# Performance work log

Measured on AMD Instinct MI355X. Metric: run time of the kernel, lower is better.

## Reference

```python
import jax, jax.numpy as jnp
import numpy as np

WS, OWS, NHEAD = 4, 6, 6          # window, overlap window = 4 + int(0.5*4), heads
B, CIN, COU, H, W = 2, 192, 192, 224, 224
MID = CIN  # r = 1


def calc_rpi_oca(ws=WS, ows=OWS):
    # relative position index between ws x ws query window and ows x ows overlapping kv window
    co = np.stack(np.meshgrid(np.arange(ws), np.arange(ws), indexing='ij')).reshape(2, -1)
    ce = np.stack(np.meshgrid(np.arange(ows), np.arange(ows), indexing='ij')).reshape(2, -1)
    rel = (ce[:, None, :] - co[:, :, None]).transpose(1, 2, 0) + (ws - 1)  # [ws*ws, ows*ows, 2], >= 0
    idx = rel[..., 0] * (ws + ows - 1) + rel[..., 1]                       # in [0, (ws+ows-1)^2)
    return jnp.asarray(idx)  # [16, 36]

RPI = calc_rpi_oca()


def conv2d(x, w, b, pad):
    out = jax.lax.conv_general_dilated(x, w, (1, 1), [(pad, pad), (pad, pad)],
                                       dimension_numbers=('NCHW', 'OIHW', 'NCHW'))
    return out + b[None, :, None, None]


def group_norm(x, g, b, groups, eps=1e-5):
    n = x.shape[0]
    xg = x.reshape(n, groups, -1)
    mu = xg.mean(-1, keepdims=True)
    var = xg.var(-1, keepdims=True)
    xn = ((xg - mu) * jax.lax.rsqrt(var + eps)).reshape(x.shape)
    return xn * g[None, :, None, None] + b[None, :, None, None]


def layer_norm(x, g, b, eps=1e-5):
    mu = x.mean(-1, keepdims=True)
    var = x.var(-1, keepdims=True)
    return (x - mu) * jax.lax.rsqrt(var + eps) * g + b


def ocab(x, h, w, ln1_g, ln1_b, qkv_w, qkv_b, rpb, proj_w, proj_b,
         ln2_g, ln2_b, fc1_w, fc1_b, fc2_w, fc2_b):
    b, _, c = x.shape
    nh, nw, d = h // WS, w // WS, c // NHEAD
    shortcut = x
    xn = layer_norm(x, ln1_g, ln1_b).reshape(b, h, w, c)
    qkv = xn @ qkv_w + qkv_b                                  # [b,h,w,3c] laid out [q|k|v]
    q = qkv[..., :c]
    kv = jnp.stack([qkv[..., c:2 * c], qkv[..., 2 * c:]])     # [2,b,h,w,c]
    # non-overlapping query windows -> [b*nwin, 16, NHEAD, d]
    qw = q.reshape(b, nh, WS, nw, WS, c).transpose(0, 1, 3, 2, 4, 5).reshape(b * nh * nw, WS * WS, NHEAD, d)
    # overlapping kv windows = Unfold(kernel=OWS, stride=WS, pad=(OWS-WS)//2)
    pad = (OWS - WS) // 2
    kvp = jnp.pad(kv, ((0, 0), (0, 0), (pad, pad), (pad, pad), (0, 0)))
    rows = (jnp.arange(nh) * WS)[:, None] + jnp.arange(OWS)[None, :]   # [nh, OWS]
    cols = (jnp.arange(nw) * WS)[:, None] + jnp.arange(OWS)[None, :]   # [nw, OWS]
    patches = kvp[:, :, rows[:, None, :, None], cols[None, :, None, :], :]  # [2,b,nh,nw,OWS,OWS,c]
    kvw = patches.reshape(2, b * nh * nw, OWS * OWS, NHEAD, d)
    kw, vw = kvw[0], kvw[1]
    attn = jnp.einsum('wqhd,wkhd->whqk', qw * (d ** -0.5), kw)  # [b*nwin, NHEAD, 16, 36]
    bias = rpb[RPI.reshape(-1)].reshape(WS * WS, OWS * OWS, NHEAD).transpose(2, 0, 1)
    attn = jax.nn.softmax(attn + bias[None], axis=-1)
    out = jnp.einsum('whqk,wkhd->wqhd', attn, vw).reshape(b, nh, nw, WS, WS, c)
    out = out.transpose(0, 1, 3, 2, 4, 5).reshape(b, h * w, c)  # window_reverse
    out = out @ proj_w + proj_b + shortcut
    xm = layer_norm(out, ln2_g, ln2_b)
    mlp = jax.nn.gelu(xm @ fc1_w + fc1_b, approximate=False) @ fc2_w + fc2_b
    return out + mlp


def atoca_forward(x, conv1_w, conv1_b, gn1_g, gn1_b, conv2_w, conv2_b, gn2_g, gn2_b,
                  conv3_w, conv3_b, ln1_g, ln1_b, qkv_w, qkv_b, rpb, proj_w, proj_b,
                  ln2_g, ln2_b, fc1_w, fc1_b, fc2_w, fc2_b):
    Bx, C, Hx, Wx = x.shape
    shortcut = x
    # raw row-major reshape, exactly as the torch code (not a spatial window partition)
    out = x.reshape(Bx * (Hx // WS) * (Wx // WS), C, WS, WS)
    out = conv2d(out, conv1_w, conv1_b, 1)
    out = jax.nn.silu(group_norm(out, gn1_g, gn1_b, NHEAD))
    out = out.transpose(0, 2, 3, 1).reshape(Bx, Hx * Wx, -1)
    out = ocab(out, Hx, Wx, ln1_g, ln1_b, qkv_w, qkv_b, rpb, proj_w, proj_b,
               ln2_g, ln2_b, fc1_w, fc1_b, fc2_w, fc2_b)
    out = out.reshape(Bx * (Hx // WS) * (Wx // WS), WS, WS, -1).transpose(0, 3, 1, 2)
    out = conv2d(out, conv2_w, conv2_b, 1)
    out = group_norm(out, gn2_g, gn2_b, NHEAD)
    out = out.reshape(Bx, -1, Hx, Wx)
    out = out + conv2d(shortcut, conv3_w, conv3_b, 0)
    return jax.nn.relu(out)


def setup_inputs() -> dict:
    key = jax.random.key(0)
    ks = iter(jax.random.split(key, 32))
    rn = lambda shape, s=0.02: (s * jax.random.normal(next(ks), shape)).astype(jnp.float32)
    return {
        'x': jax.random.normal(next(ks), (B, CIN, H, W), dtype=jnp.float32),
        'conv1_w': rn((MID, CIN, 3, 3)), 'conv1_b': rn((MID,)),
        'gn1_g': jnp.ones((MID,), jnp.float32), 'gn1_b': jnp.zeros((MID,), jnp.float32),
        'conv2_w': rn((COU, MID, 3, 3)), 'conv2_b': rn((COU,)),
        'gn2_g': jnp.ones((COU,), jnp.float32), 'gn2_b': jnp.zeros((COU,), jnp.float32),
        'conv3_w': rn((COU, CIN, 1, 1)), 'conv3_b': rn((COU,)),
        'ln1_g': jnp.ones((MID,), jnp.float32), 'ln1_b': jnp.zeros((MID,), jnp.float32),
        'qkv_w': rn((MID, 3 * MID)), 'qkv_b': rn((3 * MID,)),
        'rpb': rn(((WS + OWS - 1) ** 2, NHEAD)),
        'proj_w': rn((MID, MID)), 'proj_b': rn((MID,)),
        'ln2_g': jnp.ones((MID,), jnp.float32), 'ln2_b': jnp.zeros((MID,), jnp.float32),
        'fc1_w': rn((MID, 2 * MID)), 'fc1_b': rn((2 * MID,)),
        'fc2_w': rn((2 * MID, MID)), 'fc2_b': rn((MID,)),
    }


def reference(x, conv1_w, conv1_b, gn1_g, gn1_b, conv2_w, conv2_b, gn2_g, gn2_b,
              conv3_w, conv3_b, ln1_g, ln1_b, qkv_w, qkv_b, rpb, proj_w, proj_b,
              ln2_g, ln2_b, fc1_w, fc1_b, fc2_w, fc2_b):
    return atoca_forward(x, conv1_w, conv1_b, gn1_g, gn1_b, conv2_w, conv2_b, gn2_g, gn2_b,
                         conv3_w, conv3_b, ln1_g, ln1_b, qkv_w, qkv_b, rpb, proj_w, proj_b,
                         ln2_g, ln2_b, fc1_w, fc1_b, fc2_w, fc2_b)
```

## Files before the change

kernel.cpp:

```cpp
#include <hip/hip_runtime.h>
#include <hip/hip_bf16.h>
#include <math.h>

typedef __hip_bfloat16 bf16;
typedef __attribute__((ext_vector_type(8))) short s8v;
typedef __attribute__((ext_vector_type(4))) short s4v;
typedef __attribute__((ext_vector_type(4))) float f32x4;
typedef __attribute__((ext_vector_type(2))) _Float16 h2;

constexpr int CB   = 2;
constexpr int CH   = 224, CW = 224;
constexpr int NHW  = 56;
constexpr int NPATCH = CB * NHW * NHW;
constexpr int TOKPB  = CH * CW;
constexpr int MTOK   = CB * TOKPB;

constexpr size_t B_T0  = 0;
constexpr size_t B_P2  = B_T0 + 38535168;
constexpr size_t B_P3  = B_P2 + 115605504;
constexpr size_t B_P4  = B_P3 + 38535168;
constexpr size_t B_WF1 = B_P4 + 38535168;
constexpr size_t B_WF2 = B_WF1 + 1327104;
constexpr size_t B_W3F = B_WF2 + 1327104;
constexpr size_t B_WQ  = B_W3F + 147456;
constexpr size_t B_WP  = B_WQ + 221184;
constexpr size_t B_WG1 = B_WP + 73728;
constexpr size_t B_WG2 = B_WG1 + 147456;
constexpr size_t WS_NEEDED = B_WG2 + 147456;

__device__ __forceinline__ float ldf(const float* p) { return *p; }
__device__ __forceinline__ float ldf(const bf16* p)  { return __bfloat162float(*p); }
__device__ __forceinline__ void  stf(float* p, float v) { *p = v; }
__device__ __forceinline__ void  stf(bf16* p, float v)  { *p = __float2bfloat16(v); }
__device__ __forceinline__ unsigned short f2bf(float f) {
    unsigned u = __builtin_bit_cast(unsigned, f);
    unsigned r = (u + 0x7fffu + ((u >> 16) & 1u)) >> 16;
    return (unsigned short)r;
}
__device__ __forceinline__ float bf2f(short s) {
    unsigned u = ((unsigned)(unsigned short)s) << 16;
    return __builtin_bit_cast(float, u);
}

__global__ void build_wf_kernel(const float* __restrict__ w, short* __restrict__ wf) {
    int o = blockIdx.x * 256 + threadIdx.x;
    if (o >= 331776) return;
    int within = o & 511, frag = o >> 9;
    int l = within >> 3, j = within & 7;
    int nt = frag % 12, t2 = frag / 12, ks = t2 % 6, tap = t2 / 6;
    int co = nt * 16 + (l & 15);
    int ci = ks * 32 + (l >> 4) * 8 + j;
    wf[o] = (short)f2bf(w[(co * 192 + ci) * 9 + tap]);
}
__global__ void build_wgemm_kernel(const float* __restrict__ w, short* __restrict__ wf,
                                   int K, int N) {
    int o = blockIdx.x * 256 + threadIdx.x;
    if (o >= K * N) return;
    int j = o & 7, l = (o >> 3) & 63, f = o >> 9;
    int ntiles = N >> 4;
    int kt = f / ntiles, nt = f % ntiles;
    int k = kt * 32 + (l >> 4) * 8 + j;
    int col = nt * 16 + (l & 15);
    wf[o] = (short)f2bf(w[(size_t)k * N + col]);
}
__global__ void build_w3f_kernel(const float* __restrict__ w, short* __restrict__ wf) {
    int o = blockIdx.x * 256 + threadIdx.x;
    if (o >= 36864) return;
    int j = o & 7, l = (o >> 3) & 63, f = o >> 9;
    int kt = f / 12, ct = f % 12;
    int co = ct * 16 + (l & 15);
    int ci = kt * 32 + (l >> 4) * 8 + j;
    wf[o] = (short)f2bf(w[co * 192 + ci]);
}

template <bool FIRST>
__global__ __launch_bounds__(256, 4) void conv_mfma_kernel(
    const void* __restrict__ srcv, const short* __restrict__ wf,
    const float* __restrict__ bias, const float* __restrict__ gng,
    const float* __restrict__ gnb, bf16* __restrict__ dst)
{
    __shared__ short xs[13056];
    __shared__ float gsum[4][6], gsum2[4][6], gmu[4][6], grs[4][6];
    const int tid  = threadIdx.x;
    const int lane = tid & 63, wid = tid >> 6;
    const int n0   = blockIdx.x * 4;

    if (tid < 24) { gsum[tid / 6][tid % 6] = 0.f; gsum2[tid / 6][tid % 6] = 0.f; }
    for (int u = tid; u < 4 * 192; u += 256) {
        int q = u / 192;
        xs[q * 3264 + 3072 + (u % 192)] = 0;
    }

    if constexpr (FIRST) {
        const float4* sp = (const float4*)((const float*)srcv + (size_t)n0 * 3072);
        #pragma unroll
        for (int u = 0; u < 12; ++u) {
            int idx = u * 256 + tid;
            float4 v = sp[idx];
            int q = idx / 768;
            int li = (idx % 768) * 4;
            int ci = li >> 4, p0 = li & 15;
            float vv[4] = { v.x, v.y, v.z, v.w };
            #pragma unroll
            for (int k = 0; k < 4; ++k) {
                int row = p0 + k;
                int ba = q * 6528 + ((row * 384 + ci * 2) ^ ((row & 7) << 4));
                *(short*)((char*)xs + ba) = (short)f2bf(vv[k]);
            }
        }
    } else {
        const s8v* sp8 = (const s8v*)((const bf16*)srcv + (size_t)n0 * 3072);
        #pragma unroll
        for (int u = 0; u < 6; ++u) {
            int li = u * 256 + tid;
            int r = li / 24, ch = li % 24;
            int q = r >> 4, rl = r & 15;
            s8v val = sp8[li];
            int ba = q * 6528 + ((rl * 384 + ch * 16) ^ ((rl & 7) << 4));
            *(s8v*)((char*)xs + ba) = val;
        }
    }
    __syncthreads();

    const int ntb = wid * 3;
    const int cl  = lane & 15;
    const int kg  = lane >> 4;
    f32x4 acc[3][4];
    #pragma unroll
    for (int t = 0; t < 3; ++t) {
        float bv = bias[(ntb + t) * 16 + cl];
        #pragma unroll
        for (int q = 0; q < 4; ++q) acc[t][q] = (f32x4){ bv, bv, bv, bv };
    }

    const int pi = cl >> 2, pj = cl & 3;
    const s8v* wf8 = (const s8v*)wf;

    for (int tap = 0; tap < 9; ++tap) {
        const int di = tap / 3, dj = tap % 3;
        const int ii = pi + di - 1, jj = pj + dj - 1;
        const bool valid = (ii >= 0 && ii < 4 && jj >= 0 && jj < 4);
        const int nr  = valid ? (ii * 4 + jj) : 16;
        const int rb  = nr * 384;
        const int swz = (nr & 7) << 4;
        #pragma unroll
        for (int ks = 0; ks < 6; ++ks) {
            const s8v* bp = wf8 + (size_t)((tap * 6 + ks) * 12) * 64 + lane;
            s8v b0 = bp[(ntb + 0) * 64];
            s8v b1 = bp[(ntb + 1) * 64];
            s8v b2 = bp[(ntb + 2) * 64];
            const int inner = (rb + ks * 64 + kg * 16) ^ swz;
            #pragma unroll
            for (int q = 0; q < 4; ++q) {
                s8v a = *(const s8v*)((const char*)xs + q * 6528 + inner);
                acc[0][q] = __builtin_amdgcn_mfma_f32_16x16x32_bf16(a, b0, acc[0][q], 0, 0, 0);
                acc[1][q] = __builtin_amdgcn_mfma_f32_16x16x32_bf16(a, b1, acc[1][q], 0, 0, 0);
                acc[2][q] = __builtin_amdgcn_mfma_f32_16x16x32_bf16(a, b2, acc[2][q], 0, 0, 0);
            }
        }
    }

    #pragma unroll
    for (int t = 0; t < 3; ++t) {
        const int g = (ntb + t) >> 1;
        #pragma unroll
        for (int q = 0; q < 4; ++q) {
            f32x4 A = acc[t][q];
            float s  = A[0] + A[1] + A[2] + A[3];
            float s2 = A[0]*A[0] + A[1]*A[1] + A[2]*A[2] + A[3]*A[3];
            #pragma unroll
            for (int off = 32; off; off >>= 1) { s += __shfl_xor(s, off); s2 += __shfl_xor(s2, off); }
            if (lane == 0) { atomicAdd(&gsum[q][g], s); atomicAdd(&gsum2[q][g], s2); }
        }
    }
    __syncthreads();
    if (tid < 24) {
        int q = tid / 6, g = tid % 6;
        float mu  = gsum[q][g] * (1.f / 512.f);
        float var = gsum2[q][g] * (1.f / 512.f) - mu * mu;
        gmu[q][g] = mu; grs[q][g] = rsqrtf(var + 1e-5f);
    }
    __syncthreads();

    if constexpr (FIRST) {
        #pragma unroll
        for (int t = 0; t < 3; ++t) {
            const int co = (ntb + t) * 16 + cl, g = (ntb + t) >> 1;
            const float gg = gng[co], gb = gnb[co];
            #pragma unroll
            for (int q = 0; q < 4; ++q) {
                const float mu = gmu[q][g], rs = grs[q][g];
                bf16* op = dst + (((size_t)(n0 + q) * 16) + kg * 4) * 192 + co;
                #pragma unroll
                for (int r = 0; r < 4; ++r) {
                    float v = (acc[t][q][r] - mu) * rs * gg + gb;
                    v = v / (1.f + expf(-v));
                    op[(size_t)r * 192] = __float2bfloat16(v);
                }
            }
        }
    } else {
        #pragma unroll
        for (int t = 0; t < 3; ++t) {
            const int co = (ntb + t) * 16 + cl, g = (ntb + t) >> 1;
            const float gg = gng[co], gb = gnb[co];
            #pragma unroll
            for (int q = 0; q < 4; ++q) {
                const float mu = gmu[q][g], rs = grs[q][g];
                #pragma unroll
                for (int r = 0; r < 4; ++r) {
                    float v = (acc[t][q][r] - mu) * rs * gg + gb;
                    xs[q * 3072 + co * 16 + kg * 4 + r] = (short)f2bf(v);
                }
            }
        }
        __syncthreads();
        s4v* dp = (s4v*)(dst + (size_t)n0 * 3072);
        const s4v* sps = (const s4v*)xs;
        #pragma unroll
        for (int u = 0; u < 12; ++u) {
            dp[u * 256 + tid] = sps[u * 256 + tid];
        }
    }
}

template <typename TO, bool RES, bool GELU_ACT, bool LN>
__global__ __launch_bounds__(256) void gemm_mfma_kernel(
    const bf16* __restrict__ A, const short* __restrict__ wfb,
    const float* __restrict__ bias, const bf16* __restrict__ res,
    TO* __restrict__ out, int K, int N,
    const float* __restrict__ lng, const float* __restrict__ lnb)
{
    const int tid = threadIdx.x, lane = tid & 63, wid = tid >> 6;
    const int m0 = blockIdx.x * 128, n0 = blockIdx.y * 64;
    const int cl = lane & 15, kg = lane >> 4;
    const int ntiles = N >> 4, nt0 = n0 >> 4;

    f32x4 acc[2][4];
    #pragma unroll
    for (int nf = 0; nf < 4; ++nf) {
        float bv = bias[n0 + nf * 16 + cl];
        acc[0][nf] = (f32x4){ bv, bv, bv, bv };
        acc[1][nf] = (f32x4){ bv, bv, bv, bv };
    }

    const s8v* wf8 = (const s8v*)wfb;

    if constexpr (LN) {
        s8v af[2][6];
        const int r0 = m0 + wid * 32 + cl;
        #pragma unroll
        for (int kt = 0; kt < 6; ++kt) {
            af[0][kt] = *(const s8v*)(A + (size_t)r0 * 192 + kt * 32 + kg * 8);
            af[1][kt] = *(const s8v*)(A + (size_t)(r0 + 16) * 192 + kt * 32 + kg * 8);
        }
        #pragma unroll
        for (int r = 0; r < 2; ++r) {
            float s = 0.f, s2 = 0.f;
            #pragma unroll
            for (int kt = 0; kt < 6; ++kt)
                #pragma unroll
                for (int j = 0; j < 8; ++j) {
                    float v = bf2f(af[r][kt][j]);
                    s += v; s2 += v * v;
                }
            s  += __shfl_xor(s, 16);  s2 += __shfl_xor(s2, 16);
            s  += __shfl_xor(s, 32);  s2 += __shfl_xor(s2, 32);
            const float mu = s * (1.f / 192.f);
            const float rs = rsqrtf(s2 * (1.f / 192.f) - mu * mu + 1e-5f);
            #pragma unroll
            for (int kt = 0; kt < 6; ++kt) {
                const float* gp = lng + kt * 32 + kg * 8;
                const float* bp = lnb + kt * 32 + kg * 8;
                #pragma unroll
                for (int j = 0; j < 8; ++j) {
                    float v = (bf2f(af[r][kt][j]) - mu) * rs * gp[j] + bp[j];
                    af[r][kt][j] = (short)f2bf(v);
                }
            }
        }
        #pragma unroll
        for (int kt = 0; kt < 6; ++kt) {
            #pragma unroll
            for (int nf = 0; nf < 4; ++nf) {
                s8v b = wf8[(size_t)(kt * ntiles + nt0 + nf) * 64 + lane];
                acc[0][nf] = __builtin_amdgcn_mfma_f32_16x16x32_bf16(af[0][kt], b, acc[0][nf], 0, 0, 0);
                acc[1][nf] = __builtin_amdgcn_mfma_f32_16x16x32_bf16(af[1][kt], b, acc[1][nf], 0, 0, 0);
            }
        }
    } else {
        const int nkt = K >> 5;
        for (int kt = 0; kt < nkt; ++kt) {
            s8v a0 = *(const s8v*)(A + (size_t)(m0 + wid * 32 +      cl) * K + kt * 32 + kg * 8);
            s8v a1 = *(const s8v*)(A + (size_t)(m0 + wid * 32 + 16 + cl) * K + kt * 32 + kg * 8);
            #pragma unroll
            for (int nf = 0; nf < 4; ++nf) {
                s8v b = wf8[(size_t)(kt * ntiles + nt0 + nf) * 64 + lane];
                acc[0][nf] = __builtin_amdgcn_mfma_f32_16x16x32_bf16(a0, b, acc[0][nf], 0, 0, 0);
                acc[1][nf] = __builtin_amdgcn_mfma_f32_16x16x32_bf16(a1, b, acc[1][nf], 0, 0, 0);
            }
        }
    }

    #pragma unroll
    for (int rf = 0; rf < 2; ++rf) {
        #pragma unroll
        for (int nf = 0; nf < 4; ++nf) {
            const int col = n0 + nf * 16 + cl;
            #pragma unroll
            for (int r = 0; r < 4; ++r) {
                const int row = m0 + wid * 32 + rf * 16 + kg * 4 + r;
                float v = acc[rf][nf][r];
                if (GELU_ACT) v = 0.5f * v * (1.f + erff(v * 0.70710678118f));
                if (RES) v += ldf(&res[(size_t)row * N + col]);
                stf(&out[(size_t)row * N + col], v);
            }
        }
    }
}

constexpr int HSTR = 1160;
__global__ __launch_bounds__(128) void attn_kernel(
    const bf16* __restrict__ qkv, const float* __restrict__ rpb,
    bf16* __restrict__ out)
{
    __shared__ short kh[6 * HSTR];
    const int w = blockIdx.x;
    const int b = w / (NHW * NHW), wi = w % (NHW * NHW);
    const int nhi = wi / NHW, nwi = wi % NHW;
    const int tid = threadIdx.x;
    const int r0 = nhi * 4 - 1, c0 = nwi * 4 - 1;

    #pragma unroll
    for (int it = 0; it < 7; ++it) {
        int v = tid + it * 128;
        if (v < 864) {
            int h = v / 144, rem = v % 144, kj = rem >> 2, d0 = (rem & 3) * 8;
            int rr = r0 + kj / 6, cc = c0 + kj % 6;
            s8v kvk = { 0, 0, 0, 0, 0, 0, 0, 0 };
            if (rr >= 0 && rr < CH && cc >= 0 && cc < CW) {
                size_t base = ((size_t)((b * CH + rr) * CW + cc)) * 576 + h * 32 + d0;
                kvk = *(const s8v*)(qkv + base + 192);
            }
            s8v ko;
            #pragma unroll
            for (int e = 0; e < 8; ++e)
                ko[e] = __builtin_bit_cast(short, (_Float16)bf2f(kvk[e]));
            *(s8v*)(kh + h * HSTR + kj * 32 + d0) = ko;
        }
    }
    __syncthreads();

    if (tid < 96) {
        const int h = tid >> 4, qi = tid & 15;
        const int qr = nhi * 4 + (qi >> 2), qc = nwi * 4 + (qi & 3);
        const bf16* qp = qkv + ((size_t)((b * CH + qr) * CW + qc)) * 576 + h * 32;
        h2 qh[16];
        #pragma unroll
        for (int u = 0; u < 4; ++u) {
            s8v qv = *(const s8v*)(qp + u * 8);
            #pragma unroll
            for (int e = 0; e < 4; ++e) {
                h2 p;
                p[0] = (_Float16)bf2f(qv[2 * e]);
                p[1] = (_Float16)bf2f(qv[2 * e + 1]);
                qh[u * 4 + e] = p;
            }
        }

        float sc[36];
        const char* khb = (const char*)(kh + h * HSTR);
        #pragma unroll
        for (int kj = 0; kj < 36; ++kj) {
            const uint4* kp = (const uint4*)(khb + kj * 64);
            uint4 k0 = kp[0], k1 = kp[1], k2 = kp[2], k3 = kp[3];
            unsigned kwv[16] = { k0.x, k0.y, k0.z, k0.w, k1.x, k1.y, k1.z, k1.w,
                                 k2.x, k2.y, k2.z, k2.w, k3.x, k3.y, k3.z, k3.w };
            float a = 0.f;
            #pragma unroll
            for (int e = 0; e < 16; ++e)
                a = __builtin_amdgcn_fdot2(__builtin_bit_cast(h2, kwv[e]), qh[e], a, false);
            const int rel0 = kj / 6 - (qi >> 2) + 3;
            const int rel1 = kj % 6 - (qi & 3) + 3;
            sc[kj] = a * 0.17677669529f + rpb[(rel0 * 9 + rel1) * 6 + h];
        }
        float mx = -1e30f;
        #pragma unroll
        for (int kj = 0; kj < 36; ++kj) mx = fmaxf(mx, sc[kj]);
        float sum = 0.f;
        #pragma unroll
        for (int kj = 0; kj < 36; ++kj) { sc[kj] = expf(sc[kj] - mx); sum += sc[kj]; }
        const float inv = 1.f / sum;

        float o[32];
        #pragma unroll
        for (int d = 0; d < 32; ++d) o[d] = 0.f;
        #pragma unroll
        for (int kj = 0; kj < 36; ++kj) {
            const int rr = r0 + kj / 6, cc = c0 + kj % 6;
            if (rr < 0 || rr >= CH || cc < 0 || cc >= CW) continue;
            const uint4* vp = (const uint4*)(qkv + ((size_t)((b * CH + rr) * CW + cc)) * 576 + 384 + h * 32);
            uint4 v0 = vp[0], v1 = vp[1], v2 = vp[2], v3 = vp[3];
            unsigned vwv[16] = { v0.x, v0.y, v0.z, v0.w, v1.x, v1.y, v1.z, v1.w,
                                 v2.x, v2.y, v2.z, v2.w, v3.x, v3.y, v3.z, v3.w };
            const float p = sc[kj];
            #pragma unroll
            for (int e = 0; e < 16; ++e) {
                float lo = __builtin_bit_cast(float, vwv[e] << 16);
                float hi = __builtin_bit_cast(float, vwv[e] & 0xffff0000u);
                o[2 * e]     += p * lo;
                o[2 * e + 1] += p * hi;
            }
        }
        bf16* op = out + ((size_t)(b * TOKPB + qr * CW + qc)) * 192 + h * 32;
        #pragma unroll
        for (int u = 0; u < 8; ++u) {
            s4v pk;
            #pragma unroll
            for (int e = 0; e < 4; ++e) pk[e] = (short)f2bf(o[u * 4 + e] * inv);
            *(s4v*)((bf16*)op + u * 4) = pk;
        }
    }
}

__global__ __launch_bounds__(256, 4) void final_mfma_kernel(
    const float* __restrict__ x, const short* __restrict__ w3f,
    const float* __restrict__ b3, const bf16* __restrict__ c2,
    float* __restrict__ out)
{
    __shared__ short xs2[12288];
    const int pix0 = blockIdx.x * 64;
    const int b    = blockIdx.y;
    const int tid = threadIdx.x, lane = tid & 63, wid = tid >> 6;
    const int cl = lane & 15, kg = lane >> 4;
    const float* xb = x + (size_t)b * (192 * TOKPB);

    #pragma unroll
    for (int u = 0; u < 12; ++u) {
        int idx = u * 256 + tid;
        int ci = idx >> 4, p4 = (idx & 15) << 2;
        float4 v = *(const float4*)(xb + (size_t)ci * TOKPB + pix0 + p4);
        float vv[4] = { v.x, v.y, v.z, v.w };
        #pragma unroll
        for (int k = 0; k < 4; ++k) {
            int row = p4 + k;
            int ba = (row * 384 + ci * 2) ^ ((row & 7) << 4);
            *(short*)((char*)xs2 + ba) = (short)f2bf(vv[k]);
        }
    }
    __syncthreads();

    const int ctb = wid * 3;
    f32x4 acc[3][4] = {};
    const s8v* wf8 = (const s8v*)w3f;

    #pragma unroll
    for (int kt = 0; kt < 6; ++kt) {
        s8v a0 = wf8[(size_t)(kt * 12 + ctb + 0) * 64 + lane];
        s8v a1 = wf8[(size_t)(kt * 12 + ctb + 1) * 64 + lane];
        s8v a2 = wf8[(size_t)(kt * 12 + ctb + 2) * 64 + lane];
        #pragma unroll
        for (int pt = 0; pt < 4; ++pt) {
            int row = pt * 16 + cl;
            int ba = (row * 384 + kt * 64 + kg * 16) ^ ((row & 7) << 4);
            s8v bfr = *(const s8v*)((const char*)xs2 + ba);
            acc[0][pt] = __builtin_amdgcn_mfma_f32_16x16x32_bf16(a0, bfr, acc[0][pt], 0, 0, 0);
            acc[1][pt] = __builtin_amdgcn_mfma_f32_16x16x32_bf16(a1, bfr, acc[1][pt], 0, 0, 0);
            acc[2][pt] = __builtin_amdgcn_mfma_f32_16x16x32_bf16(a2, bfr, acc[2][pt], 0, 0, 0);
        }
    }

    #pragma unroll
    for (int t = 0; t < 3; ++t) {
        #pragma unroll
        for (int r = 0; r < 4; ++r) {
            const int co = (ctb + t) * 16 + kg * 4 + r;
            const float bb = b3[co];
            const size_t rowbase = (size_t)b * (192 * TOKPB) + (size_t)co * TOKPB + pix0;
            #pragma unroll
            for (int pt = 0; pt < 4; ++pt) {
                const size_t f = rowbase + pt * 16 + cl;
                float v = acc[t][pt][r] + bb + bf2f(__builtin_bit_cast(short, c2[f]));
                out[f] = fmaxf(v, 0.f);
            }
        }
    }
}

extern "C" void kernel_launch(void* const* d_in, const int* in_sizes, int n_in,
                              void* d_out, int out_size, void* d_ws, size_t ws_size,
                              hipStream_t stream)
{
    if (ws_size < WS_NEEDED) return;

    const float* x       = (const float*)d_in[0];
    const float* conv1_w = (const float*)d_in[1];
    const float* conv1_b = (const float*)d_in[2];
    const float* gn1_g   = (const float*)d_in[3];
    const float* gn1_b   = (const float*)d_in[4];
    const float* conv2_w = (const float*)d_in[5];
    const float* conv2_b = (const float*)d_in[6];
    const float* gn2_g   = (const float*)d_in[7];
    const float* gn2_b   = (const float*)d_in[8];
    const float* conv3_w = (const float*)d_in[9];
    const float* conv3_b = (const float*)d_in[10];
    const float* ln1_g   = (const float*)d_in[11];
    const float* ln1_b   = (const float*)d_in[12];
    const float* qkv_w   = (const float*)d_in[13];
    const float* qkv_b   = (const float*)d_in[14];
    const float* rpb     = (const float*)d_in[15];
    const float* proj_w  = (const float*)d_in[16];
    const float* proj_b  = (const float*)d_in[17];
    const float* ln2_g   = (const float*)d_in[18];
    const float* ln2_b   = (const float*)d_in[19];
    const float* fc1_w   = (const float*)d_in[20];
    const float* fc1_b   = (const float*)d_in[21];
    const float* fc2_w   = (const float*)d_in[22];
    const float* fc2_b   = (const float*)d_in[23];

    char* wsb = (char*)d_ws;
    bf16*  T0  = (bf16*)(wsb + B_T0);
    bf16*  P2  = (bf16*)(wsb + B_P2);
    bf16*  P3  = (bf16*)(wsb + B_P3);
    bf16*  P4  = (bf16*)(wsb + B_P4);
    short* WF1 = (short*)(wsb + B_WF1);
    short* WF2 = (short*)(wsb + B_WF2);
    short* W3F = (short*)(wsb + B_W3F);
    short* WQ  = (short*)(wsb + B_WQ);
    short* WP  = (short*)(wsb + B_WP);
    short* WG1 = (short*)(wsb + B_WG1);
    short* WG2 = (short*)(wsb + B_WG2);
    float* OUT = (float*)d_out;

    build_wf_kernel<<<(331776 + 255) / 256, 256, 0, stream>>>(conv1_w, WF1);
    build_wf_kernel<<<(331776 + 255) / 256, 256, 0, stream>>>(conv2_w, WF2);
    build_w3f_kernel<<<(36864 + 255) / 256, 256, 0, stream>>>(conv3_w, W3F);
    build_wgemm_kernel<<<(110592 + 255) / 256, 256, 0, stream>>>(qkv_w, WQ, 192, 576);
    build_wgemm_kernel<<<(36864 + 255) / 256, 256, 0, stream>>>(proj_w, WP, 192, 192);
    build_wgemm_kernel<<<(73728 + 255) / 256, 256, 0, stream>>>(fc1_w, WG1, 192, 384);
    build_wgemm_kernel<<<(73728 + 255) / 256, 256, 0, stream>>>(fc2_w, WG2, 384, 192);

    conv_mfma_kernel<true><<<NPATCH / 4, 256, 0, stream>>>(x, WF1, conv1_b, gn1_g, gn1_b, T0);
    gemm_mfma_kernel<bf16, false, false, true><<<dim3(MTOK / 128, 9), 256, 0, stream>>>(
        T0, WQ, qkv_b, nullptr, P2, 192, 576, ln1_g, ln1_b);
    attn_kernel<<<NPATCH, 128, 0, stream>>>(P2, rpb, P3);
    gemm_mfma_kernel<bf16, true, false, false><<<dim3(MTOK / 128, 3), 256, 0, stream>>>(
        P3, WP, proj_b, T0, P4, 192, 192, nullptr, nullptr);
    gemm_mfma_kernel<bf16, false, true, true><<<dim3(MTOK / 128, 6), 256, 0, stream>>>(
        P4, WG1, fc1_b, nullptr, P2, 192, 384, ln2_g, ln2_b);
    gemm_mfma_kernel<bf16, true, false, false><<<dim3(MTOK / 128, 3), 256, 0, stream>>>(
        P2, WG2, fc2_b, P4, P3, 384, 192, nullptr, nullptr);
    conv_mfma_kernel<false><<<NPATCH / 4, 256, 0, stream>>>(P3, WF2, conv2_b, gn2_g, gn2_b, P4);
    final_mfma_kernel<<<dim3(TOKPB / 64, CB), 256, 0, stream>>>(x, W3F, conv3_b, P4, OUT);
}
```

Measured before the change: 620.1 us.

## Emit QKV as head-major fp16 planes and stage V in shared memory

```diff
diff --git a/kernel.cpp b/kernel.cpp
--- a/kernel.cpp
+++ b/kernel.cpp
@@ -14,6 +14,7 @@
 constexpr int NPATCH = CB * NHW * NHW;
 constexpr int TOKPB  = CH * CW;
 constexpr int MTOK   = CB * TOKPB;
+constexpr size_t SECSZ = 19267584;
 
 constexpr size_t B_T0  = 0;
 constexpr size_t B_P2  = B_T0 + 38535168;
@@ -224,7 +225,7 @@
     }
 }
 
-template <typename TO, bool RES, bool GELU_ACT, bool LN>
+template <typename TO, bool RES, bool GELU_ACT, bool LN, bool QKVOUT>
 __global__ __launch_bounds__(256) void gemm_mfma_kernel(
     const bf16* __restrict__ A, const short* __restrict__ wfb,
     const float* __restrict__ bias, const bf16* __restrict__ res,
@@ -313,7 +314,15 @@
                 float v = acc[rf][nf][r];
                 if (GELU_ACT) v = 0.5f * v * (1.f + erff(v * 0.70710678118f));
                 if (RES) v += ldf(&res[(size_t)row * N + col]);
-                stf(&out[(size_t)row * N + col], v);
+                if constexpr (QKVOUT) {
+                    const int sec = n0 / 192;
+                    const int c = col - sec * 192, h = c >> 5, d = c & 31;
+                    const int bb2 = row / TOKPB, t = row - bb2 * TOKPB;
+                    ((_Float16*)out)[(size_t)sec * SECSZ +
+                        ((size_t)(bb2 * 6 + h) * TOKPB + t) * 32 + d] = (_Float16)v;
+                } else {
+                    stf(&out[(size_t)row * N + col], v);
+                }
             }
         }
     }
@@ -321,32 +330,34 @@
 
 constexpr int HSTR = 1160;
 __global__ __launch_bounds__(128) void attn_kernel(
-    const bf16* __restrict__ qkv, const float* __restrict__ rpb,
+    const _Float16* __restrict__ qf, const float* __restrict__ rpb,
     bf16* __restrict__ out)
 {
     __shared__ short kh[6 * HSTR];
+    __shared__ short vh[6 * HSTR];
     const int w = blockIdx.x;
     const int b = w / (NHW * NHW), wi = w % (NHW * NHW);
     const int nhi = wi / NHW, nwi = wi % NHW;
     const int tid = threadIdx.x;
     const int r0 = nhi * 4 - 1, c0 = nwi * 4 - 1;
-
-    #pragma unroll
-    for (int it = 0; it < 7; ++it) {
+    const _Float16* kfb = qf + SECSZ;
+    const _Float16* vfb = qf + 2 * SECSZ;
+
+    #pragma unroll
+    for (int it = 0; it < 14; ++it) {
         int v = tid + it * 128;
-        if (v < 864) {
-            int h = v / 144, rem = v % 144, kj = rem >> 2, d0 = (rem & 3) * 8;
+        if (v < 1728) {
+            int kv = v >= 864 ? 1 : 0;
+            int u = v - kv * 864;
+            int h = u / 144, rem = u % 144, kj = rem >> 2, d0 = (rem & 3) * 8;
             int rr = r0 + kj / 6, cc = c0 + kj % 6;
-            s8v kvk = { 0, 0, 0, 0, 0, 0, 0, 0 };
+            s8v val = { 0, 0, 0, 0, 0, 0, 0, 0 };
             if (rr >= 0 && rr < CH && cc >= 0 && cc < CW) {
-                size_t base = ((size_t)((b * CH + rr) * CW + cc)) * 576 + h * 32 + d0;
-                kvk = *(const s8v*)(qkv + base + 192);
-            }
-            s8v ko;
-            #pragma unroll
-            for (int e = 0; e < 8; ++e)
-                ko[e] = __builtin_bit_cast(short, (_Float16)bf2f(kvk[e]));
-            *(s8v*)(kh + h * HSTR + kj * 32 + d0) = ko;
+                const _Float16* src = kv ? vfb : kfb;
+                val = *(const s8v*)(src + ((size_t)(b * 6 + h) * TOKPB + rr * CW + cc) * 32 + d0);
+            }
+            short* dst = kv ? vh : kh;
+            *(s8v*)(dst + h * HSTR + kj * 32 + d0) = val;
         }
     }
     __syncthreads();
@@ -354,70 +365,71 @@
     if (tid < 96) {
         const int h = tid >> 4, qi = tid & 15;
         const int qr = nhi * 4 + (qi >> 2), qc = nwi * 4 + (qi & 3);
-        const bf16* qp = qkv + ((size_t)((b * CH + qr) * CW + qc)) * 576 + h * 32;
+        const _Float16* qp = qf + ((size_t)(b * 6 + h) * TOKPB + qr * CW + qc) * 32;
         h2 qh[16];
         #pragma unroll
         for (int u = 0; u < 4; ++u) {
-            s8v qv = *(const s8v*)(qp + u * 8);
-            #pragma unroll
-            for (int e = 0; e < 4; ++e) {
-                h2 p;
-                p[0] = (_Float16)bf2f(qv[2 * e]);
-                p[1] = (_Float16)bf2f(qv[2 * e + 1]);
-                qh[u * 4 + e] = p;
-            }
+            uint4 qa = *(const uint4*)(qp + u * 8);
+            qh[u * 4 + 0] = __builtin_bit_cast(h2, qa.x);
+            qh[u * 4 + 1] = __builtin_bit_cast(h2, qa.y);
+            qh[u * 4 + 2] = __builtin_bit_cast(h2, qa.z);
+            qh[u * 4 + 3] = __builtin_bit_cast(h2, qa.w);
         }
 
         float sc[36];
-        const char* khb = (const char*)(kh + h * HSTR);
+        const short* khb = kh + h * HSTR;
         #pragma unroll
         for (int kj = 0; kj < 36; ++kj) {
-            const uint4* kp = (const uint4*)(khb + kj * 64);
+            const uint4* kp = (const uint4*)(khb + kj * 32);
             uint4 k0 = kp[0], k1 = kp[1], k2 = kp[2], k3 = kp[3];
             unsigned kwv[16] = { k0.x, k0.y, k0.z, k0.w, k1.x, k1.y, k1.z, k1.w,
                                  k2.x, k2.y, k2.z, k2.w, k3.x, k3.y, k3.z, k3.w };
-            float a = 0.f;
-            #pragma unroll
-            for (int e = 0; e < 16; ++e)
-                a = __builtin_amdgcn_fdot2(__builtin_bit_cast(h2, kwv[e]), qh[e], a, false);
+            float a0 = 0.f, a1 = 0.f, a2 = 0.f, a3 = 0.f;
+            #pragma unroll
+            for (int e = 0; e < 4; ++e) {
+                a0 = __builtin_amdgcn_fdot2(__builtin_bit_cast(h2, kwv[4*e+0]), qh[4*e+0], a0, false);
+                a1 = __builtin_amdgcn_fdot2(__builtin_bit_cast(h2, kwv[4*e+1]), qh[4*e+1], a1, false);
+                a2 = __builtin_amdgcn_fdot2(__builtin_bit_cast(h2, kwv[4*e+2]), qh[4*e+2], a2, false);
+                a3 = __builtin_amdgcn_fdot2(__builtin_bit_cast(h2, kwv[4*e+3]), qh[4*e+3], a3, false);
+            }
             const int rel0 = kj / 6 - (qi >> 2) + 3;
             const int rel1 = kj % 6 - (qi & 3) + 3;
-            sc[kj] = a * 0.17677669529f + rpb[(rel0 * 9 + rel1) * 6 + h];
+            sc[kj] = ((a0 + a1) + (a2 + a3)) * 0.17677669529f + rpb[(rel0 * 9 + rel1) * 6 + h];
         }
         float mx = -1e30f;
         #pragma unroll
         for (int kj = 0; kj < 36; ++kj) mx = fmaxf(mx, sc[kj]);
         float sum = 0.f;
         #pragma unroll
-        for (int kj = 0; kj < 36; ++kj) { sc[kj] = expf(sc[kj] - mx); sum += sc[kj]; }
+        for (int kj = 0; kj < 36; ++kj) { sc[kj] = __expf(sc[kj] - mx); sum += sc[kj]; }
         const float inv = 1.f / sum;
 
-        float o[32];
-        #pragma unroll
-        for (int d = 0; d < 32; ++d) o[d] = 0.f;
+        h2 o2[16];
+        #pragma unroll
+        for (int e = 0; e < 16; ++e) o2[e] = (h2){ (_Float16)0.f, (_Float16)0.f };
+        const short* vhb = vh + h * HSTR;
         #pragma unroll
         for (int kj = 0; kj < 36; ++kj) {
-            const int rr = r0 + kj / 6, cc = c0 + kj % 6;
-            if (rr < 0 || rr >= CH || cc < 0 || cc >= CW) continue;
-            const uint4* vp = (const uint4*)(qkv + ((size_t)((b * CH + rr) * CW + cc)) * 576 + 384 + h * 32);
+            const uint4* vp = (const uint4*)(vhb + kj * 32);
             uint4 v0 = vp[0], v1 = vp[1], v2 = vp[2], v3 = vp[3];
             unsigned vwv[16] = { v0.x, v0.y, v0.z, v0.w, v1.x, v1.y, v1.z, v1.w,
                                  v2.x, v2.y, v2.z, v2.w, v3.x, v3.y, v3.z, v3.w };
-            const float p = sc[kj];
-            #pragma unroll
-            for (int e = 0; e < 16; ++e) {
-                float lo = __builtin_bit_cast(float, vwv[e] << 16);
-                float hi = __builtin_bit_cast(float, vwv[e] & 0xffff0000u);
-                o[2 * e]     += p * lo;
-                o[2 * e + 1] += p * hi;
-            }
+            const _Float16 ph = (_Float16)sc[kj];
+            const h2 ph2 = { ph, ph };
+            #pragma unroll
+            for (int e = 0; e < 16; ++e)
+                o2[e] = __builtin_bit_cast(h2, vwv[e]) * ph2 + o2[e];
         }
         bf16* op = out + ((size_t)(b * TOKPB + qr * CW + qc)) * 192 + h * 32;
         #pragma unroll
         for (int u = 0; u < 8; ++u) {
             s4v pk;
             #pragma unroll
-            for (int e = 0; e < 4; ++e) pk[e] = (short)f2bf(o[u * 4 + e] * inv);
+            for (int e = 0; e < 2; ++e) {
+                h2 ov = o2[u * 2 + e];
+                pk[2 * e]     = (short)f2bf((float)ov[0] * inv);
+                pk[2 * e + 1] = (short)f2bf((float)ov[1] * inv);
+            }
             *(s4v*)((bf16*)op + u * 4) = pk;
         }
     }
@@ -520,7 +532,8 @@
 
     char* wsb = (char*)d_ws;
     bf16*  T0  = (bf16*)(wsb + B_T0);
-    bf16*  P2  = (bf16*)(wsb + B_P2);
+    _Float16* QF = (_Float16*)(wsb + B_P2);
+    bf16*  HID = (bf16*)(wsb + B_P2);
     bf16*  P3  = (bf16*)(wsb + B_P3);
     bf16*  P4  = (bf16*)(wsb + B_P4);
     short* WF1 = (short*)(wsb + B_WF1);
@@ -541,15 +554,15 @@
     build_wgemm_kernel<<<(73728 + 255) / 256, 256, 0, stream>>>(fc2_w, WG2, 384, 192);
 
     conv_mfma_kernel<true><<<NPATCH / 4, 256, 0, stream>>>(x, WF1, conv1_b, gn1_g, gn1_b, T0);
-    gemm_mfma_kernel<bf16, false, false, true><<<dim3(MTOK / 128, 9), 256, 0, stream>>>(
-        T0, WQ, qkv_b, nullptr, P2, 192, 576, ln1_g, ln1_b);
-    attn_kernel<<<NPATCH, 128, 0, stream>>>(P2, rpb, P3);
-    gemm_mfma_kernel<bf16, true, false, false><<<dim3(MTOK / 128, 3), 256, 0, stream>>>(
+    gemm_mfma_kernel<_Float16, false, false, true, true><<<dim3(MTOK / 128, 9), 256, 0, stream>>>(
+        T0, WQ, qkv_b, nullptr, QF, 192, 576, ln1_g, ln1_b);
+    attn_kernel<<<NPATCH, 128, 0, stream>>>(QF, rpb, P3);
+    gemm_mfma_kernel<bf16, true, false, false, false><<<dim3(MTOK / 128, 3), 256, 0, stream>>>(
         P3, WP, proj_b, T0, P4, 192, 192, nullptr, nullptr);
-    gemm_mfma_kernel<bf16, false, true, true><<<dim3(MTOK / 128, 6), 256, 0, stream>>>(
-        P4, WG1, fc1_b, nullptr, P2, 192, 384, ln2_g, ln2_b);
-    gemm_mfma_kernel<bf16, true, false, false><<<dim3(MTOK / 128, 3), 256, 0, stream>>>(
-        P2, WG2, fc2_b, P4, P3, 384, 192, nullptr, nullptr);
+    gemm_mfma_kernel<bf16, false, true, true, false><<<dim3(MTOK / 128, 6), 256, 0, stream>>>(
+        P4, WG1, fc1_b, nullptr, HID, 192, 384, ln2_g, ln2_b);
+    gemm_mfma_kernel<bf16, true, false, false, false><<<dim3(MTOK / 128, 3), 256, 0, stream>>>(
+        HID, WG2, fc2_b, P4, P3, 384, 192, nullptr, nullptr);
     conv_mfma_kernel<false><<<NPATCH / 4, 256, 0, stream>>>(P3, WF2, conv2_b, gn2_g, gn2_b, P4);
     final_mfma_kernel<<<dim3(TOKPB / 64, CB), 256, 0, stream>>>(x, W3F, conv3_b, P4, OUT);
 }
```

New measurement: 606.9 us. -2.1%, faster.
